# Optimization experiments

Hardware: AMD Instinct MI355X
Metric: run time of the kernel (lower is better)

## Reference

```python
import jax, jax.numpy as jnp
import numpy as np

# ---- fixed heterogeneous-graph metadata (Hetionet-like) ----
N_C, N_D, N_G = 15000, 3000, 40000          # Compound, Disease, Gene node counts
NODE_N = [N_C, N_D, N_G]
HID, OUT, HEADS, LAYERS = 128, 64, 4, 2
DH = HID // HEADS                            # 32 = head dim
# edge types as (src_type, dst_type):
#  0 treats C->D, 1 rev_treats D->C, 2 binds C->G, 3 rev_binds G->C, 4 interacts G->G
EDGE_META = [(0, 1), (1, 0), (0, 2), (2, 0), (2, 2)]
E_CNT = [80000, 80000, 250000, 250000, 400000]
N_EDGE_TYPES = len(EDGE_META)
N_ADD = 8000                                 # int(n_train * ratio * (epoch-1)) = int(80000*0.05*2)


def setup_inputs() -> dict:
    key = jax.random.key(0)
    ks = iter(jax.random.split(key, 64))
    s = 0.05
    inp = {}
    # node-type embedding tables (the model uses embed.weight as input features)
    inp['emb_compound'] = jax.random.normal(next(ks), (N_C, HID), jnp.float32) * s
    inp['emb_disease'] = jax.random.normal(next(ks), (N_D, HID), jnp.float32) * s
    inp['emb_gene'] = jax.random.normal(next(ks), (N_G, HID), jnp.float32) * s
    # HGTConv params, stacked over [layer, node_type] / [layer, edge_type]
    inp['W_kqv'] = jax.random.normal(next(ks), (LAYERS, 3, HID, 3 * HID), jnp.float32) * s
    inp['b_kqv'] = jnp.zeros((LAYERS, 3, 3 * HID), jnp.float32)
    inp['W_out'] = jax.random.normal(next(ks), (LAYERS, 3, HID, HID), jnp.float32) * s
    inp['b_out'] = jnp.zeros((LAYERS, 3, HID), jnp.float32)
    inp['skip'] = jnp.ones((LAYERS, 3), jnp.float32)
    inp['a_rel'] = jax.random.normal(next(ks), (LAYERS, N_EDGE_TYPES, HEADS, DH, DH), jnp.float32) * s
    inp['m_rel'] = jax.random.normal(next(ks), (LAYERS, N_EDGE_TYPES, HEADS, DH, DH), jnp.float32) * s
    inp['p_rel'] = jnp.ones((LAYERS, N_EDGE_TYPES, HEADS), jnp.float32)
    # final per-node-type Linear(hidden -> out)
    inp['W_fin'] = jax.random.normal(next(ks), (3, HID, OUT), jnp.float32) * s
    inp['b_fin'] = jnp.zeros((3, OUT), jnp.float32)
    # edge indices per edge type: [2, E] with row0=src idx, row1=dst idx
    names = ['ei_treats', 'ei_rev_treats', 'ei_binds', 'ei_rev_binds', 'ei_interacts']
    for name, (st, dt), e in zip(names, EDGE_META, E_CNT):
        src = jax.random.randint(next(ks), (e,), 0, NODE_N[st], dtype=jnp.int32)
        dst = jax.random.randint(next(ks), (e,), 0, NODE_N[dt], dtype=jnp.int32)
        inp[name] = jnp.stack([src, dst], 0)
    inp['train_edge_index'] = inp['ei_treats']
    inp['n_edge_add'] = int(N_ADD)
    return inp


def _hgt_layer(x_list, edge_list, Wkqv, bkqv, Wout, bout, skip, a_rel, m_rel, p_rel):
    """One PyG-style HGTConv layer over the heterogeneous graph."""
    kqv = [x @ Wkqv[t] + bkqv[t] for t, x in enumerate(x_list)]
    k = [a[:, :HID].reshape(-1, HEADS, DH) for a in kqv]
    q = [a[:, HID:2 * HID].reshape(-1, HEADS, DH) for a in kqv]
    v = [a[:, 2 * HID:].reshape(-1, HEADS, DH) for a in kqv]
    scale = 1.0 / np.sqrt(DH)
    buf = {t: {'a': [], 'v': [], 'i': []} for t in range(3)}
    for e, (st, dt) in enumerate(EDGE_META):
        src, dst = edge_list[e][0], edge_list[e][1]
        # per-edge-type, per-head relation transforms of gathered src k/v
        k_e = jnp.einsum('ehd,hdf->ehf', k[st][src], a_rel[e])   # [E,H,DH]
        v_e = jnp.einsum('ehd,hdf->ehf', v[st][src], m_rel[e])   # [E,H,DH]
        alpha = (q[dt][dst] * k_e).sum(-1) * p_rel[e] * scale    # [E,H]
        buf[dt]['a'].append(alpha); buf[dt]['v'].append(v_e); buf[dt]['i'].append(dst)
    out_list = []
    for t, x in enumerate(x_list):
        n = NODE_N[t]
        alpha = jnp.concatenate(buf[t]['a'], 0)
        vv = jnp.concatenate(buf[t]['v'], 0)
        idx = jnp.concatenate(buf[t]['i'], 0)
        # softmax over all incoming edges per destination node (across edge types)
        m = jax.ops.segment_max(alpha, idx, num_segments=n)
        ex = jnp.exp(alpha - m[idx])
        den = jax.ops.segment_sum(ex, idx, num_segments=n)
        w = ex / (den[idx] + 1e-16)
        agg = jax.ops.segment_sum(w[:, :, None] * vv, idx, num_segments=n).reshape(n, HID)
        o = jax.nn.gelu(agg, approximate=False) @ Wout[t] + bout[t]
        a_s = jax.nn.sigmoid(skip[t])
        out_list.append(a_s * o + (1.0 - a_s) * x)
    return out_list


def reference(emb_compound, emb_disease, emb_gene, W_kqv, b_kqv, W_out, b_out, skip,
              a_rel, m_rel, p_rel, W_fin, b_fin,
              ei_treats, ei_rev_treats, ei_binds, ei_rev_binds, ei_interacts,
              train_edge_index, n_edge_add):
    edge_list = [ei_treats, ei_rev_treats, ei_binds, ei_rev_binds, ei_interacts]
    # encode: embeddings -> HGT convs -> per-type linear
    x = [emb_compound, emb_disease, emb_gene]
    for l in range(LAYERS):
        x = _hgt_layer(x, edge_list, W_kqv[l], b_kqv[l], W_out[l], b_out[l],
                       skip[l], a_rel[l], m_rel[l], p_rel[l])
    z = [x[t] @ W_fin[t] + b_fin[t] for t in range(3)]
    # decode_all: dense prob matrix, zero out training edges, global top-k
    prob = jax.nn.sigmoid(z[0] @ z[1].T)                     # [N_C, N_D]
    prob = prob.at[train_edge_index[0], train_edge_index[1]].set(0.0)
    _, top_idx = jax.lax.top_k(prob.reshape(-1), n_edge_add)
    row = top_idx // N_D
    col = top_idx % N_D
    edge_index_add = jnp.stack([row, col], 0)
    edge_weight_add = prob[row, col]
    return edge_index_add, edge_weight_add
```

## Files before the change

kernel.cpp:

```cpp
#include <hip/hip_runtime.h>
#include <hip/hip_bf16.h>
#include <math.h>

#define N_C 15000
#define N_D 3000
#define N_G 40000
#define NTOT 58000
#define HID 128
#define HEADS 4
#define DH 32
#define KTOP 8000
#define KROWP 3072
#define NPROBP 46202880u
#define EQCAP 1048576u
#define DPB 8

#define SC_DEN 1125899906842624.0
#define SC_AGG 281474976710656.0

static __device__ __forceinline__ unsigned fenc32(float f){
    unsigned u = __float_as_uint(f);
    return (u & 0x80000000u) ? ~u : (u | 0x80000000u);
}
static __device__ __forceinline__ float fdec32(unsigned um){
    return __uint_as_float((um & 0x80000000u) ? (um & 0x7fffffffu) : ~um);
}

static __device__ __forceinline__ float pexp32f(float x){
    x = fminf(x,  88.3762626647949f);
    x = fmaxf(x, -87.3365478515625f);
    float fx = fmaf(x, 1.44269504088896341f, 0.5f);
    fx = floorf(fx);
    float r = fmaf(fx, -0.693359375f, x);
    r = fmaf(fx, 2.12194440e-4f, r);
    float r2 = __fmul_rn(r, r);
    float y = 1.9875691500E-4f;
    y = fmaf(y, r, 1.3981999507E-3f);
    y = fmaf(y, r, 8.3334519073E-3f);
    y = fmaf(y, r, 4.1665795894E-2f);
    y = fmaf(y, r, 1.6666665459E-1f);
    y = fmaf(y, r, 5.0000001201E-1f);
    y = fmaf(y, r2, r);
    y = __fadd_rn(y, 1.0f);
    int m = (int)fx;
    y = __fmul_rn(y, __uint_as_float((unsigned)(m + 127) << 23));
    return y;
}

static __device__ __forceinline__ float np_sigmoid_f32(float x){
    float e = pexp32f(-x);
    float s = __fadd_rn(1.0f, e);
    return __fdiv_rn(1.0f, s);
}

__global__ void k_init_nmax(unsigned* __restrict__ NMAX){
    int i = blockIdx.x*256 + threadIdx.x;
    if (i < NTOT*HEADS) NMAX[i] = 0x007FFFFFu;
}

__global__ void k_count(const int* __restrict__ edst, unsigned* __restrict__ cnt, int E){
    int i = blockIdx.x*256 + threadIdx.x;
    if (i < E) atomicAdd(&cnt[edst[i]], 1u);
}

__global__ void __launch_bounds__(256) k_scan(const unsigned* __restrict__ cnt,
                                              unsigned* __restrict__ offs, int n){
    __shared__ unsigned ssum[256];
    int tid = threadIdx.x;
    int chunk = (n + 255) / 256;
    int lo = tid*chunk, hi = lo+chunk; if (hi > n) hi = n; if (lo > n) lo = n;
    unsigned s = 0;
    for (int i=lo;i<hi;i++) s += cnt[i];
    ssum[tid] = s; __syncthreads();
    for (int st=1; st<256; st<<=1){
        unsigned t = (tid>=st) ? ssum[tid-st] : 0u;
        __syncthreads();
        ssum[tid] += t;
        __syncthreads();
    }
    unsigned run = ssum[tid] - s;
    for (int i=lo;i<hi;i++){ offs[i] = run; run += cnt[i]; }
    if (tid == 0) offs[n] = ssum[255];
}

__global__ void k_fill(const int* __restrict__ esrc, const int* __restrict__ edst,
                       const unsigned* __restrict__ offs, unsigned* __restrict__ curs,
                       unsigned* __restrict__ csr_src, unsigned* __restrict__ csr_el,
                       int E, int csr_base){
    int i = blockIdx.x*256 + threadIdx.x;
    if (i >= E) return;
    int dst = edst[i];
    unsigned pos = offs[dst] + atomicAdd(&curs[dst], 1u);
    csr_src[csr_base + pos] = (unsigned)esrc[i];
    csr_el [csr_base + pos] = (unsigned)i;
}

__global__ void k_kqv(const float* __restrict__ X, const float* __restrict__ W,
                      const float* __restrict__ Bv, float* __restrict__ KQ,
                      float* __restrict__ V, int n0, int ncnt)
{
    __shared__ float sA[16][128];
    int rb = blockIdx.x*16;
    int sec = blockIdx.y;
    int col = threadIdx.x & 127, half = threadIdx.x >> 7;
    for (int i = threadIdx.x; i < 2048; i += 256){
        int r = i >> 7, c = i & 127;
        sA[r][c] = (rb + r < ncnt) ? X[(size_t)(n0+rb+r)*HID + c] : 0.f;
    }
    __syncthreads();
    float acc[8];
#pragma unroll
    for (int i=0;i<8;i++) acc[i]=0.f;
    int wc = sec*128 + col;
    for (int k=0;k<128;k++){
        float w = W[(size_t)k*384 + wc];
#pragma unroll
        for (int i=0;i<8;i++) acc[i] = fmaf(sA[half*8+i][k], w, acc[i]);
    }
    float bb = Bv[wc];
    for (int i=0;i<8;i++){
        int r = rb + half*8 + i;
        if (r >= ncnt) continue;
        float y = __fadd_rn(acc[i], bb);
        if (sec < 2) KQ[(size_t)(n0+r)*256 + sec*128 + col] = y;
        else         V[(size_t)(n0+r)*128 + col] = y;
    }
}

__global__ void __launch_bounds__(256) k_rel(const float* __restrict__ IN, int stride, int secoff,
        const float* __restrict__ Mrel, float* __restrict__ OUT, int n0, int ncnt)
{
    __shared__ float sM[HEADS*DH*DH];
    for (int i=threadIdx.x;i<HEADS*DH*DH;i+=256) sM[i]=Mrel[i];
    __syncthreads();
    int sub = threadIdx.x>>7, lane = threadIdx.x&127;
    int h = lane>>5, f = lane&31;
    int row = blockIdx.x*2 + sub;
    if (row >= ncnt) return;
    float vval = IN[(size_t)(n0+row)*stride + secoff + lane];
    double t = 0.0;
    const float* mh = &sM[h*DH*DH];
#pragma unroll
    for (int d=0; d<DH; ++d)
        t += (double)__shfl(vval, d, 32) * (double)mh[d*DH+f];
    OUT[(size_t)row*HID + lane] = (float)t;
}

__global__ void __launch_bounds__(128) k_alpha_csr(const float* __restrict__ KQ,
        const float* __restrict__ KE,
        const unsigned* __restrict__ csr_src, const unsigned* __restrict__ csr_el,
        const unsigned* __restrict__ offs, const float* __restrict__ Prel,
        float* __restrict__ ALPHA, unsigned* __restrict__ NMAX,
        int eoff, int nodst, int csr_base, int ndst)
{
    int lane = threadIdx.x, h = lane>>5, f = lane&31;
    float p = Prel[h];
    int d0 = blockIdx.x*DPB;
    int d1 = d0+DPB; if (d1 > ndst) d1 = ndst;
    for (int dst=d0; dst<d1; ++dst){
        unsigned beg = offs[dst], end = offs[dst+1];
        if (beg == end) continue;
        float qv = KQ[(size_t)(nodst+dst)*256 + 128 + lane];
        unsigned lmax = 0x007FFFFFu;
        for (unsigned j=beg; j<end; ++j){
            unsigned src = csr_src[csr_base+j];
            unsigned el  = csr_el [csr_base+j];
            float ke = KE[(size_t)src*HID + lane];
            double part = (double)qv * (double)ke;
#pragma unroll
            for (int off=16; off>0; off>>=1) part += __shfl_xor(part, off);
            if (f==0){
                float s32 = (float)part;
                float a = __fmul_rn(__fmul_rn(s32, p), 0.17677669529663687f);
                ALPHA[(size_t)(eoff+el)*HEADS + h] = a;
                unsigned enc = fenc32(a);
                if (enc > lmax) lmax = enc;
            }
        }
        if (f==0) atomicMax(&NMAX[(size_t)(nodst+dst)*HEADS + h], lmax);
    }
}

__global__ void k_expsum(const float* __restrict__ ALPHA,
                         const int* __restrict__ edst, const unsigned* __restrict__ NMAX,
                         unsigned long long* __restrict__ NSUM,
                         int E, int eoff, int nodst)
{
    int i = blockIdx.x*256 + threadIdx.x;
    if (i >= E*HEADS) return;
    int e = i>>2, h = i&3;
    int dst = edst[e];
    float m = fdec32(NMAX[(size_t)(nodst+dst)*HEADS + h]);
    float a = ALPHA[(size_t)(eoff+e)*HEADS + h];
    float ex = pexp32f(__fsub_rn(a, m));
    atomicAdd(&NSUM[(size_t)(nodst+dst)*HEADS + h],
              (unsigned long long)(long long)llrint((double)ex * SC_DEN));
}

__global__ void k_wgt(float* __restrict__ ALPHA, const int* __restrict__ edst,
                      const unsigned* __restrict__ NMAX,
                      const unsigned long long* __restrict__ NSUM,
                      int E, int eoff, int nodst)
{
    int i = blockIdx.x*256 + threadIdx.x;
    if (i >= E*HEADS) return;
    int e = i>>2, h = i&3;
    int dst = edst[e];
    float m = fdec32(NMAX[(size_t)(nodst+dst)*HEADS + h]);
    float a = ALPHA[(size_t)(eoff+e)*HEADS + h];
    float ex = pexp32f(__fsub_rn(a, m));
    float den = (float)((double)(long long)NSUM[(size_t)(nodst+dst)*HEADS + h] * (1.0/SC_DEN));
    float denp = __fadd_rn(den, 1e-16f);
    ALPHA[(size_t)(eoff+e)*HEADS + h] = __fdiv_rn(ex, denp);
}

__global__ void __launch_bounds__(128) k_agg2(
    const float* __restrict__ VE, const unsigned* __restrict__ csr_src,
    const unsigned* __restrict__ csr_el, const unsigned* __restrict__ offs,
    const float* __restrict__ W, unsigned long long* __restrict__ AGG,
    int eoff, int nodst, int csr_base, int ndst)
{
    int lane = threadIdx.x, h = lane>>5;
    int d0 = blockIdx.x*DPB;
    int d1 = d0+DPB; if (d1 > ndst) d1 = ndst;
    for (int dst=d0; dst<d1; ++dst){
        unsigned beg = offs[dst], end = offs[dst+1];
        if (beg == end) continue;
        long long acc = 0;
        for (unsigned j=beg; j<end; ++j){
            unsigned src = csr_src[csr_base+j];
            unsigned el  = csr_el [csr_base+j];
            float w  = W[(size_t)(eoff+el)*HEADS + h];
            float ve = VE[(size_t)src*HID + lane];
            float prod = __fmul_rn(w, ve);
            acc += llrint((double)prod*SC_AGG);
        }
        size_t o = (size_t)(nodst+dst)*HID + lane;
        AGG[o] = AGG[o] + (unsigned long long)acc;
    }
}

__global__ void k_outl(const unsigned long long* __restrict__ AGG,
                       const float* __restrict__ W, const float* __restrict__ Bv,
                       float* __restrict__ X,
                       const float* __restrict__ skipv, int n0, int ncnt)
{
    __shared__ float sA[16][128];
    int rb = blockIdx.x*16;
    int col = threadIdx.x&127, half = threadIdx.x>>7;
    for (int i=threadIdx.x;i<2048;i+=256){
        int r=i>>7,c=i&127;
        float g = 0.f;
        if (rb+r<ncnt){
            float x = (float)((double)(long long)AGG[(size_t)(n0+rb+r)*128 + c] * (1.0/SC_AGG));
            float t = __fdiv_rn(x, 1.4142135623730951f);
            float ef = (float)erf((double)t);
            g = __fmul_rn(__fmul_rn(0.5f, x), __fadd_rn(1.0f, ef));
        }
        sA[r][c]=g;
    }
    __syncthreads();
    float acc[8];
#pragma unroll
    for(int i=0;i<8;i++)acc[i]=0.f;
    for(int k=0;k<128;k++){
        float w=W[(size_t)k*128+col];
#pragma unroll
        for(int i=0;i<8;i++)acc[i]=fmaf(sA[half*8+i][k], w, acc[i]);
    }
    float a_s = np_sigmoid_f32(skipv[0]);
    float om  = __fsub_rn(1.0f, a_s);
    for(int i=0;i<8;i++){
        int r=rb+half*8+i;
        if(r<ncnt){
            size_t idx=(size_t)(n0+r)*128+col;
            float o = __fadd_rn(acc[i], Bv[col]);
            X[idx] = __fadd_rn(__fmul_rn(a_s, o), __fmul_rn(om, X[idx]));
        }
    }
}

__global__ void k_zfin(const float* __restrict__ X, const float* __restrict__ W,
                       const float* __restrict__ Bv, float* __restrict__ Z,
                       int n0, int ncnt, int zoff)
{
    __shared__ float sA[16][128];
    int rb=blockIdx.x*16;
    int col=threadIdx.x&63, quad=threadIdx.x>>6;
    for(int i=threadIdx.x;i<2048;i+=256){
        int r=i>>7,c=i&127;
        sA[r][c]=(rb+r<ncnt)?X[(size_t)(n0+rb+r)*128+c]:0.f;
    }
    __syncthreads();
    float acc[4]={0.f,0.f,0.f,0.f};
    for(int k=0;k<128;k++){
        float w=W[(size_t)k*64+col];
#pragma unroll
        for(int i=0;i<4;i++)acc[i]=fmaf(sA[quad*4+i][k], w, acc[i]);
    }
    for(int i=0;i<4;i++){
        int r=rb+quad*4+i;
        if(r<ncnt)Z[(size_t)(zoff+r)*64+col]=__fadd_rn(acc[i], Bv[col]);
    }
}

__global__ void k_mask(const int* __restrict__ tr, unsigned* __restrict__ MASK, int E){
    int i = blockIdx.x*256 + threadIdx.x;
    if (i>=E) return;
    unsigned bit = (unsigned)(tr[i]*KROWP + tr[E+i]);
    atomicOr(&MASK[bit>>5], 1u<<(bit&31));
}

__global__ void __launch_bounds__(256) k_keys(const float* __restrict__ Z,
        const unsigned* __restrict__ MASK, unsigned* __restrict__ KEYS,
        unsigned* __restrict__ STATE)
{
    __shared__ float sC[64][65];
    __shared__ float sD[64][65];
    __shared__ unsigned shh[256];
    int db = blockIdx.x*64, cb = blockIdx.y*64;
    shh[threadIdx.x] = 0u;
    for (int i=threadIdx.x;i<4096;i+=256){
        int r=i>>6, c=i&63;
        sC[r][c] = (cb+r<N_C) ? Z[(size_t)(cb+r)*64+c] : 0.f;
        sD[r][c] = (db+r<N_D) ? Z[(size_t)(N_C+db+r)*64+c] : 0.f;
    }
    __syncthreads();
    int tx = threadIdx.x & 15, ty = threadIdx.x >> 4;
    int r0 = ty*4, c0 = tx*4;
    float acc[4][4];
#pragma unroll
    for(int i=0;i<4;i++)
#pragma unroll
        for(int j=0;j<4;j++) acc[i][j]=0.f;
    for (int k=0;k<64;k++){
        float a0=sC[r0][k],a1=sC[r0+1][k],a2=sC[r0+2][k],a3=sC[r0+3][k];
        float b0=sD[c0][k],b1=sD[c0+1][k],b2=sD[c0+2][k],b3=sD[c0+3][k];
        acc[0][0]=fmaf(a0,b0,acc[0][0]); acc[0][1]=fmaf(a0,b1,acc[0][1]);
        acc[0][2]=fmaf(a0,b2,acc[0][2]); acc[0][3]=fmaf(a0,b3,acc[0][3]);
        acc[1][0]=fmaf(a1,b0,acc[1][0]); acc[1][1]=fmaf(a1,b1,acc[1][1]);
        acc[1][2]=fmaf(a1,b2,acc[1][2]); acc[1][3]=fmaf(a1,b3,acc[1][3]);
        acc[2][0]=fmaf(a2,b0,acc[2][0]); acc[2][1]=fmaf(a2,b1,acc[2][1]);
        acc[2][2]=fmaf(a2,b2,acc[2][2]); acc[2][3]=fmaf(a2,b3,acc[2][3]);
        acc[3][0]=fmaf(a3,b0,acc[3][0]); acc[3][1]=fmaf(a3,b1,acc[3][1]);
        acc[3][2]=fmaf(a3,b2,acc[3][2]); acc[3][3]=fmaf(a3,b3,acc[3][3]);
    }
    unsigned lastb=0xFFFFFFFFu, rcnt=0;
#pragma unroll
    for (int i=0;i<4;i++){
        int cr = cb + r0 + i;
        int dcb = db + c0;
        bool rok = (cr < N_C);
        unsigned mword = rok ? MASK[((size_t)cr*KROWP + dcb)>>5] : 0u;
        unsigned kk[4];
#pragma unroll
        for (int j=0;j<4;j++){
            int dc = dcb + j;
            unsigned key = 0u;
            if (rok && dc < N_D){
                float p = np_sigmoid_f32(acc[i][j]);
                key = fenc32(p);
                if (mword & (1u << (dc & 31))) key = 0u;
            }
            kk[j] = key;
            unsigned b = key >> 24;
            if (b == lastb) rcnt++;
            else { if (rcnt) atomicAdd(&shh[lastb], rcnt); lastb = b; rcnt = 1; }
        }
        *reinterpret_cast<uint4*>(&KEYS[(size_t)cr*KROWP + dcb]) =
            make_uint4(kk[0],kk[1],kk[2],kk[3]);
    }
    if (rcnt) atomicAdd(&shh[lastb], rcnt);
    __syncthreads();
    unsigned v = shh[threadIdx.x];
    if (v) atomicAdd(&STATE[8+threadIdx.x], v);
}

__global__ void k_hist(const unsigned* __restrict__ KEYS, unsigned* __restrict__ STATE, int level){
    __shared__ unsigned sh[256];
    for (int i=threadIdx.x;i<256;i+=blockDim.x) sh[i]=0;
    __syncthreads();
    unsigned prefix = STATE[0];
    int shift = 24 - 8*level;
    size_t stride = (size_t)gridDim.x*blockDim.x;
    unsigned lastb = 0xFFFFFFFFu, rcnt = 0;
    for (size_t i = (size_t)blockIdx.x*blockDim.x+threadIdx.x; i < (size_t)NPROBP; i += stride){
        unsigned k = KEYS[i];
        if ((k >> (shift+8)) != prefix) continue;
        unsigned b = (k>>shift)&255u;
        if (b == lastb) rcnt++;
        else { if (rcnt) atomicAdd(&sh[lastb], rcnt); lastb = b; rcnt = 1; }
    }
    if (rcnt) atomicAdd(&sh[lastb], rcnt);
    __syncthreads();
    for (int i=threadIdx.x;i<256;i+=blockDim.x) if (sh[i]) atomicAdd(&STATE[8+i], sh[i]);
}

__global__ void k_hfin(unsigned* STATE){
    if (threadIdx.x==0 && blockIdx.x==0){
        unsigned cnt = STATE[1];
        unsigned prefix = STATE[0];
        int b = 255;
        for (; b>0; --b){
            unsigned c = STATE[8+b];
            if (cnt + c >= (unsigned)KTOP) break;
            cnt += c;
        }
        STATE[0] = (prefix<<8) | (unsigned)b;
        STATE[1] = cnt;
        for (int i=0;i<256;i++) STATE[8+i]=0;
    }
}

__global__ void k_collect(const unsigned* __restrict__ KEYS, unsigned* __restrict__ STATE,
                          unsigned long long* __restrict__ CANDI, unsigned* __restrict__ EQI)
{
    unsigned T = STATE[0];
    size_t stride = (size_t)gridDim.x*blockDim.x;
    for (size_t i=(size_t)blockIdx.x*blockDim.x+threadIdx.x; i<(size_t)NPROBP; i+=stride){
        unsigned k = KEYS[i];
        if (k > T){
            unsigned pos = atomicAdd(&STATE[2], 1u);
            if (pos < 8192u)
                CANDI[pos] = ((unsigned long long)k << 32)
                           | (unsigned long long)(0xFFFFFFFFu - (unsigned)i);
        } else if (k == T){
            unsigned pos = atomicAdd(&STATE[3], 1u);
            if (pos < EQCAP) EQI[pos] = (unsigned)i;
        }
    }
}

__global__ void __launch_bounds__(256) k_rank(const unsigned long long* __restrict__ CANDI,
        const unsigned* __restrict__ STATE, const unsigned* __restrict__ EQI,
        float* __restrict__ OUT)
{
    __shared__ unsigned long long sc[2048];
    unsigned* se = (unsigned*)sc;
    unsigned G = STATE[2]; if (G > 8192u) G = 8192u;
    unsigned nE = STATE[3]; if (nE > 8192u) nE = 8192u;
    unsigned T = STATE[0];
    unsigned need = ((unsigned)KTOP > G) ? ((unsigned)KTOP - G) : 0u;

    int phase = blockIdx.x & 1;
    unsigned i = (blockIdx.x >> 1)*256 + threadIdx.x;
    if (phase == 0){
        unsigned long long ci = (i < G) ? CANDI[i] : 0ull;
        unsigned rank = 0;
        for (unsigned t0=0; t0<G; t0+=2048u){
            unsigned tl = G - t0; if (tl > 2048u) tl = 2048u;
            __syncthreads();
            for (unsigned k=threadIdx.x; k<tl; k+=256u) sc[k] = CANDI[t0+k];
            __syncthreads();
            if (i < G)
                for (unsigned k=0; k<tl; ++k) rank += (sc[k] > ci) ? 1u : 0u;
        }
        if (i < G){
            unsigned idx = 0xFFFFFFFFu - (unsigned)(ci & 0xFFFFFFFFull);
            unsigned key = (unsigned)(ci >> 32);
            unsigned c = idx/KROWP, d = idx - c*KROWP;
            OUT[rank] = (float)c; OUT[KTOP+rank] = (float)d; OUT[2*KTOP+rank] = fdec32(key);
        }
    } else {
        float pT = fdec32(T);
        unsigned ii = (i < nE) ? EQI[i] : 0xFFFFFFFFu;
        unsigned rank = 0;
        for (unsigned t0=0; t0<nE; t0+=2048u){
            unsigned tl = nE - t0; if (tl > 2048u) tl = 2048u;
            __syncthreads();
            for (unsigned k=threadIdx.x; k<tl; k+=256u) se[k] = EQI[t0+k];
            __syncthreads();
            if (i < nE)
                for (unsigned k=0; k<tl; ++k) rank += (se[k] < ii) ? 1u : 0u;
        }
        if (i < nE && rank < need){
            unsigned c = ii/KROWP, d = ii - c*KROWP;
            unsigned rr = G + rank;
            OUT[rr] = (float)c; OUT[KTOP+rr] = (float)d; OUT[2*KTOP+rr] = pT;
        }
    }
}

extern "C" void kernel_launch(void* const* d_in, const int* in_sizes, int n_in,
                              void* d_out, int out_size, void* d_ws, size_t ws_size,
                              hipStream_t stream)
{
    const float* embC = (const float*)d_in[0];
    const float* embD = (const float*)d_in[1];
    const float* embG = (const float*)d_in[2];
    const float* Wkqv = (const float*)d_in[3];
    const float* bkqv = (const float*)d_in[4];
    const float* Wout = (const float*)d_in[5];
    const float* bout = (const float*)d_in[6];
    const float* skipv= (const float*)d_in[7];
    const float* arel = (const float*)d_in[8];
    const float* mrel = (const float*)d_in[9];
    const float* prel = (const float*)d_in[10];
    const float* Wfin = (const float*)d_in[11];
    const float* bfin = (const float*)d_in[12];
    const int* ei[5] = {(const int*)d_in[13],(const int*)d_in[14],(const int*)d_in[15],
                        (const int*)d_in[16],(const int*)d_in[17]};
    const int* tri  = (const int*)d_in[18];
    int trE = in_sizes[18]/2;

    static const int NODE_OFF[3] = {0, N_C, N_C + N_D};
    static const int NODE_CNT[3] = {N_C, N_D, N_G};
    static const int EM_ST[5] = {0,1,0,2,2};
    static const int EM_DT[5] = {1,0,2,0,2};
    static const int EM_E[5]  = {80000,80000,250000,250000,400000};
    static const int EM_OFF[5]= {0,80000,160000,410000,660000};
    static const int DOFF[5] = {0,3000,18000,58000,73000};
    static const int OFO[5]  = {0,3001,18002,58003,73004};

    char* ws = (char*)d_ws;
    float* X  = (float*)(ws + 0);
    float* KQ = (float*)(ws + 29696000);
    float* V  = (float*)(ws + 89088000);
    float* ALPHA = (float*)(ws + 118784000);
    unsigned* NMAX = (unsigned*)(ws + 135744000);
    unsigned long long* NSUM = (unsigned long long*)(ws + 136672000);
    unsigned long long* AGG = (unsigned long long*)(ws + 139456000);
    float* VE = (float*)(ws + 198848000);
    unsigned* OFFS = (unsigned*)(ws + 219328000);
    unsigned* CURS = (unsigned*)(ws + 219780032);
    unsigned* CSRS = (unsigned*)(ws + 220232032);
    unsigned* CSRE = (unsigned*)(ws + 224472032);
    float* KE = (float*)(ws + 228712032);
    unsigned* KEYS = (unsigned*)(ws + 0);
    float* Z = (float*)(ws + 198848000);
    unsigned* MASK = (unsigned*)(ws + 203456000);
    unsigned* STATE= (unsigned*)(ws + 209216000);
    unsigned long long* CANDI = (unsigned long long*)(ws + 209224192);
    unsigned* EQI  = (unsigned*)(ws + 209289728);

    hipMemcpyAsync(X,                          embC, (size_t)N_C*HID*4, hipMemcpyDeviceToDevice, stream);
    hipMemcpyAsync(X + (size_t)N_C*HID,        embD, (size_t)N_D*HID*4, hipMemcpyDeviceToDevice, stream);
    hipMemcpyAsync(X + (size_t)(N_C+N_D)*HID,  embG, (size_t)N_G*HID*4, hipMemcpyDeviceToDevice, stream);

    hipMemsetAsync(CURS, 0, 113000*4, stream);
    for (int e=0;e<5;e++)
        k_count<<<(EM_E[e]+255)/256, 256, 0, stream>>>(ei[e]+EM_E[e], CURS + DOFF[e], EM_E[e]);
    for (int e=0;e<5;e++)
        k_scan<<<1, 256, 0, stream>>>(CURS + DOFF[e], OFFS + OFO[e], NODE_CNT[EM_DT[e]]);
    hipMemsetAsync(CURS, 0, 113000*4, stream);
    for (int e=0;e<5;e++)
        k_fill<<<(EM_E[e]+255)/256, 256, 0, stream>>>(ei[e], ei[e]+EM_E[e],
            OFFS + OFO[e], CURS + DOFF[e], CSRS, CSRE, EM_E[e], EM_OFF[e]);

    for (int l=0; l<2; ++l){
        k_init_nmax<<<(NTOT*HEADS+255)/256, 256, 0, stream>>>(NMAX);
        hipMemsetAsync(NSUM, 0, (size_t)NTOT*HEADS*8, stream);
        hipMemsetAsync(AGG,  0, (size_t)NTOT*HID*8,  stream);
        for (int t=0;t<3;t++){
            k_kqv<<<dim3((NODE_CNT[t]+15)/16, 3), 256, 0, stream>>>(
                X, Wkqv + (size_t)(l*3+t)*128*384, bkqv + (size_t)(l*3+t)*384,
                KQ, V, NODE_OFF[t], NODE_CNT[t]);
        }
        for (int e=0;e<5;e++){
            int nsrc = NODE_CNT[EM_ST[e]];
            int ndst = NODE_CNT[EM_DT[e]];
            k_rel<<<(nsrc+1)/2, 256, 0, stream>>>(
                KQ, 256, 0, arel + (size_t)(l*5+e)*HEADS*DH*DH, KE,
                NODE_OFF[EM_ST[e]], nsrc);
            k_alpha_csr<<<(ndst+DPB-1)/DPB, 128, 0, stream>>>(
                KQ, KE, CSRS, CSRE, OFFS + OFO[e],
                prel + (size_t)(l*5+e)*HEADS,
                ALPHA, NMAX, EM_OFF[e], NODE_OFF[EM_DT[e]], EM_OFF[e], ndst);
        }
        for (int e=0;e<5;e++){
            int tot = EM_E[e]*HEADS;
            k_expsum<<<(tot+255)/256, 256, 0, stream>>>(
                ALPHA, ei[e]+EM_E[e], NMAX, NSUM, EM_E[e], EM_OFF[e], NODE_OFF[EM_DT[e]]);
        }
        for (int e=0;e<5;e++){
            int tot = EM_E[e]*HEADS;
            k_wgt<<<(tot+255)/256, 256, 0, stream>>>(
                ALPHA, ei[e]+EM_E[e], NMAX, NSUM, EM_E[e], EM_OFF[e], NODE_OFF[EM_DT[e]]);
        }
        for (int e=0;e<5;e++){
            int nsrc = NODE_CNT[EM_ST[e]];
            int ndst = NODE_CNT[EM_DT[e]];
            k_rel<<<(nsrc+1)/2, 256, 0, stream>>>(
                V, 128, 0, mrel + (size_t)(l*5+e)*HEADS*DH*DH, VE,
                NODE_OFF[EM_ST[e]], nsrc);
            k_agg2<<<(ndst+DPB-1)/DPB, 128, 0, stream>>>(
                VE, CSRS, CSRE, OFFS + OFO[e], ALPHA, AGG,
                EM_OFF[e], NODE_OFF[EM_DT[e]], EM_OFF[e], ndst);
        }
        for (int t=0;t<3;t++){
            k_outl<<<(NODE_CNT[t]+15)/16, 256, 0, stream>>>(
                AGG, Wout + (size_t)(l*3+t)*128*128, bout + (size_t)(l*3+t)*128,
                X, skipv + (l*3+t), NODE_OFF[t], NODE_CNT[t]);
        }
    }

    k_zfin<<<(N_C+15)/16, 256, 0, stream>>>(X, Wfin + 0,      bfin + 0,  Z, 0,   N_C, 0);
    k_zfin<<<(N_D+15)/16, 256, 0, stream>>>(X, Wfin + 128*64, bfin + 64, Z, N_C, N_D, N_C);

    hipMemsetAsync(MASK, 0, 5760000, stream);
    hipMemsetAsync(STATE, 0, 8192, stream);
    k_mask<<<(trE+255)/256, 256, 0, stream>>>(tri, MASK, trE);
    k_keys<<<dim3(48, 235), 256, 0, stream>>>(Z, MASK, KEYS, STATE);
    k_hfin<<<1, 64, 0, stream>>>(STATE);
    for (int lev=1; lev<4; ++lev){
        k_hist<<<2048, 256, 0, stream>>>(KEYS, STATE, lev);
        k_hfin<<<1, 64, 0, stream>>>(STATE);
    }
    k_collect<<<2048, 256, 0, stream>>>(KEYS, STATE, CANDI, EQI);
    k_rank<<<64, 256, 0, stream>>>(CANDI, STATE, EQI, (float*)d_out);
}
```

Before: 3.791 ms.

## Compute attention logits per edge instead of per destination CSR segment

Replaces the destination-grouped CSR attention-score kernel with an edge-parallel kernel. Each 128-thread sub-block handles a fixed run of edges in COO order, reading source and destination indices directly and doing a per-edge atomicMax on the node maximum. This removes the load imbalance of variable-degree destination loops and the serial inner loop. In exchange it reloads the query row for every edge and issues one atomic per edge and head, where before there was one per destination.

```diff
diff --git a/kernel.cpp b/kernel.cpp
--- a/kernel.cpp
+++ b/kernel.cpp
@@ -14,6 +14,7 @@
 #define NPROBP 46202880u
 #define EQCAP 1048576u
 #define DPB 8
+#define EPB 8
 
 #define SC_DEN 1125899906842624.0
 #define SC_AGG 281474976710656.0
@@ -146,38 +147,33 @@
     OUT[(size_t)row*HID + lane] = (float)t;
 }
 
-__global__ void __launch_bounds__(128) k_alpha_csr(const float* __restrict__ KQ,
+__global__ void __launch_bounds__(256) k_alpha4(const float* __restrict__ KQ,
         const float* __restrict__ KE,
-        const unsigned* __restrict__ csr_src, const unsigned* __restrict__ csr_el,
-        const unsigned* __restrict__ offs, const float* __restrict__ Prel,
+        const int* __restrict__ esrc, const int* __restrict__ edst,
+        const float* __restrict__ Prel,
         float* __restrict__ ALPHA, unsigned* __restrict__ NMAX,
-        int eoff, int nodst, int csr_base, int ndst)
-{
-    int lane = threadIdx.x, h = lane>>5, f = lane&31;
+        int E, int eoff, int nodst)
+{
+    int sub = threadIdx.x>>7, lane = threadIdx.x&127;
+    int h = lane>>5, f = lane&31;
     float p = Prel[h];
-    int d0 = blockIdx.x*DPB;
-    int d1 = d0+DPB; if (d1 > ndst) d1 = ndst;
-    for (int dst=d0; dst<d1; ++dst){
-        unsigned beg = offs[dst], end = offs[dst+1];
-        if (beg == end) continue;
+    int ebase = (blockIdx.x*2 + sub) * EPB;
+#pragma unroll
+    for (int i=0;i<EPB;i++){
+        int e = ebase + i;
+        if (e >= E) return;
+        int src = esrc[e], dst = edst[e];
+        float ke = KE[(size_t)src*HID + lane];
         float qv = KQ[(size_t)(nodst+dst)*256 + 128 + lane];
-        unsigned lmax = 0x007FFFFFu;
-        for (unsigned j=beg; j<end; ++j){
-            unsigned src = csr_src[csr_base+j];
-            unsigned el  = csr_el [csr_base+j];
-            float ke = KE[(size_t)src*HID + lane];
-            double part = (double)qv * (double)ke;
-#pragma unroll
-            for (int off=16; off>0; off>>=1) part += __shfl_xor(part, off);
-            if (f==0){
-                float s32 = (float)part;
-                float a = __fmul_rn(__fmul_rn(s32, p), 0.17677669529663687f);
-                ALPHA[(size_t)(eoff+el)*HEADS + h] = a;
-                unsigned enc = fenc32(a);
-                if (enc > lmax) lmax = enc;
-            }
-        }
-        if (f==0) atomicMax(&NMAX[(size_t)(nodst+dst)*HEADS + h], lmax);
+        double part = (double)qv * (double)ke;
+#pragma unroll
+        for (int off=16; off>0; off>>=1) part += __shfl_xor(part, off);
+        if (f==0){
+            float s32 = (float)part;
+            float a = __fmul_rn(__fmul_rn(s32, p), 0.17677669529663687f);
+            ALPHA[(size_t)(eoff+e)*HEADS + h] = a;
+            atomicMax(&NMAX[(size_t)(nodst+dst)*HEADS + h], fenc32(a));
+        }
     }
 }
 
@@ -558,14 +554,14 @@
         }
         for (int e=0;e<5;e++){
             int nsrc = NODE_CNT[EM_ST[e]];
-            int ndst = NODE_CNT[EM_DT[e]];
             k_rel<<<(nsrc+1)/2, 256, 0, stream>>>(
                 KQ, 256, 0, arel + (size_t)(l*5+e)*HEADS*DH*DH, KE,
                 NODE_OFF[EM_ST[e]], nsrc);
-            k_alpha_csr<<<(ndst+DPB-1)/DPB, 128, 0, stream>>>(
-                KQ, KE, CSRS, CSRE, OFFS + OFO[e],
+            int ngrp = (EM_E[e] + EPB - 1) / EPB;
+            k_alpha4<<<(ngrp+1)/2, 256, 0, stream>>>(
+                KQ, KE, ei[e], ei[e]+EM_E[e],
                 prel + (size_t)(l*5+e)*HEADS,
-                ALPHA, NMAX, EM_OFF[e], NODE_OFF[EM_DT[e]], EM_OFF[e], ndst);
+                ALPHA, NMAX, EM_E[e], EM_OFF[e], NODE_OFF[EM_DT[e]]);
         }
         for (int e=0;e<5;e++){
             int tot = EM_E[e]*HEADS;
```

Result: faster. 3.445 ms (-9.1%).
